# Performance work log

Measured on AMD Instinct MI355X. Metric: run time of the kernel, lower is better.

The kernel has to match this reference:

```python
import jax, jax.numpy as jnp
import numpy as np

WS = 7        # window size (square)
SH = 3        # shift size
NH = 8        # num heads
N = WS * WS   # tokens per window


def _rel_pos_index():
    coords = np.stack(np.meshgrid(np.arange(WS), np.arange(WS), indexing='ij'))
    cf = coords.reshape(2, -1)                      # (2, N)
    rel = cf[:, :, None] - cf[:, None, :]           # (2, N, N)
    rel = rel.transpose(1, 2, 0)
    rel[:, :, 0] += WS - 1
    rel[:, :, 1] += WS - 1
    rel[:, :, 0] *= 2 * WS - 1
    return rel.sum(-1)                              # (N, N) int


def _attn_mask(pH, pW):
    img = np.zeros((pH, pW), dtype=np.float32)
    h_sl = [(0, pH - WS), (pH - WS, pH - SH), (pH - SH, pH)]
    w_sl = [(0, pW - WS), (pW - WS, pW - SH), (pW - SH, pW)]
    cnt = 0
    for h0, h1 in h_sl:
        for w0, w1 in w_sl:
            img[h0:h1, w0:w1] = cnt
            cnt += 1
    m = img.reshape(pH // WS, WS, pW // WS, WS).transpose(0, 2, 1, 3).reshape(-1, N)
    diff = m[:, None, :] - m[:, :, None]            # (nw, N, N)
    return np.where(diff != 0, -100.0, 0.0).astype(np.float32)


def setup_inputs() -> dict:
    key = jax.random.key(0)
    ks = jax.random.split(key, 6)
    C = 256
    return {
        'x': jax.random.normal(ks[0], (32, 56, 56, C), dtype=jnp.float32),
        'qkv_weight': jax.random.normal(ks[1], (3 * C, C), dtype=jnp.float32) * 0.02,
        'qkv_bias': jax.random.normal(ks[2], (3 * C,), dtype=jnp.float32) * 0.02,
        'proj_weight': jax.random.normal(ks[3], (C, C), dtype=jnp.float32) * 0.02,
        'proj_bias': jax.random.normal(ks[4], (C,), dtype=jnp.float32) * 0.02,
        'rpb_table': jax.random.normal(ks[5], ((2 * WS - 1) ** 2, NH), dtype=jnp.float32) * 0.02,
    }


def reference(x, qkv_weight, qkv_bias, proj_weight, proj_bias, rpb_table):
    B, H, W, C = x.shape
    hd = C // NH
    pad_r = (WS - W % WS) % WS
    pad_b = (WS - H % WS) % WS
    xp = jnp.pad(x, ((0, 0), (0, pad_b), (0, pad_r), (0, 0)))
    pH, pW = H + pad_b, W + pad_r
    xp = jnp.roll(xp, shift=(-SH, -SH), axis=(1, 2))
    nw = (pH // WS) * (pW // WS)
    # window partition -> (B*nw, N, C)
    xw = xp.reshape(B, pH // WS, WS, pW // WS, WS, C)
    xw = xw.transpose(0, 1, 3, 2, 4, 5).reshape(B * nw, N, C)
    # qkv projection
    qkv = xw @ qkv_weight.T + qkv_bias                      # (B*nw, N, 3C)
    qkv = qkv.reshape(B * nw, N, 3, NH, hd).transpose(2, 0, 3, 1, 4)
    q, k, v = qkv[0], qkv[1], qkv[2]                        # (B*nw, NH, N, hd)
    q = q * (hd ** -0.5)
    attn = jnp.einsum('bhnd,bhmd->bhnm', q, k)              # (B*nw, NH, N, N)
    # relative position bias
    idx = jnp.asarray(_rel_pos_index())
    bias = rpb_table[idx].transpose(2, 0, 1)                # (NH, N, N)
    attn = attn + bias[None]
    # shift mask
    mask = jnp.asarray(_attn_mask(pH, pW))                  # (nw, N, N)
    attn = attn.reshape(B, nw, NH, N, N) + mask[None, :, None]
    attn = jax.nn.softmax(attn.reshape(B * nw, NH, N, N), axis=-1)
    out = jnp.einsum('bhnm,bhmd->bhnd', attn, v)            # (B*nw, NH, N, hd)
    out = out.transpose(0, 2, 1, 3).reshape(B * nw, N, C)
    out = out @ proj_weight.T + proj_bias
    # window reverse
    out = out.reshape(B, pH // WS, pW // WS, WS, WS, C)
    out = out.transpose(0, 1, 3, 2, 4, 5).reshape(B, pH, pW, C)
    out = jnp.roll(out, shift=(SH, SH), axis=(1, 2))
    return out[:, :H, :W, :]
```

## Files before the change

### kernel.cpp

```cpp
#include <hip/hip_runtime.h>
#include <hip/hip_bf16.h>

typedef __attribute__((ext_vector_type(4))) float f32x4;
typedef __attribute__((ext_vector_type(8))) short s16x8;
typedef __attribute__((ext_vector_type(4))) short s16x4;
typedef __attribute__((ext_vector_type(4))) unsigned uintx4;

#define LBS 264
#define VTS 72
#define LOS 132

__device__ __forceinline__ unsigned cvt2bf(float a, float b) {
    unsigned r;
    asm("v_cvt_pk_bf16_f32 %0, %1, %2" : "=v"(r) : "v"(a), "v"(b));
    return r;
}

__device__ __forceinline__ s16x4 pk4bf(float a, float b, float c, float d) {
    uint2 t = { cvt2bf(a, b), cvt2bf(c, d) };
    return __builtin_bit_cast(s16x4, t);
}

__device__ __forceinline__ s16x8 expand_z(s16x4 c) {
    uint2 u = __builtin_bit_cast(uint2, c);
    uintx4 r = { u.x & 0xFFFFu, u.x >> 16, u.y & 0xFFFFu, u.y >> 16 };
    return __builtin_bit_cast(s16x8, r);
}

__global__ void wcvt_kernel(const float* __restrict__ qw, const float* __restrict__ pw,
                            short* __restrict__ wqkv, short* __restrict__ wproj) {
    int idx = blockIdx.x * blockDim.x + threadIdx.x;
    int stride = gridDim.x * blockDim.x;
    for (int i = idx; i < 65536; i += stride) {
        const float* src = (i < 49152) ? (qw + i * 4) : (pw + (i - 49152) * 4);
        unsigned* dst = (unsigned*)((i < 49152) ? (wqkv + i * 4) : (wproj + (i - 49152) * 4));
        const f32x4 v = *(const f32x4*)src;
        uint2 o = { cvt2bf(v.x, v.y), cvt2bf(v.z, v.w) };
        *(uint2*)dst = o;
    }
}

__global__ void bmgen_kernel(const float* __restrict__ rpb, float* __restrict__ bm) {
    int idx = blockIdx.x * blockDim.x + threadIdx.x;
    if (idx >= 131072) return;
    int j = idx & 63;
    int i = (idx >> 6) & 63;
    int h = (idx >> 12) & 7;
    int c = idx >> 15;
    int cy = c >> 1, cx = c & 1;
    float v;
    if (j >= 49) {
        v = -1e9f;
    } else {
        int ic = i > 48 ? 48 : i;
        int yi = ic / 7, xi = ic % 7;
        int yj = j / 7, xj = j % 7;
        float bias = rpb[((yi - yj + 6) * 13 + (xi - xj + 6)) * 8 + h];
        int ri = (cy ? (yi < 4 ? 1 : 2) : 0) * 3 + (cx ? (xi < 4 ? 1 : 2) : 0);
        int rj = (cy ? (yj < 4 ? 1 : 2) : 0) * 3 + (cx ? (xj < 4 ? 1 : 2) : 0);
        float mask = (ri != rj) ? -100.0f : 0.0f;
        v = (bias + mask) * 1.4426950408889634f;
    }
    bm[idx] = v;
}

__global__ __launch_bounds__(512, 4)
void attn_kernel(const float* __restrict__ x,
                 const float* __restrict__ qkv_bias,
                 const short* __restrict__ wqkv,
                 const float* __restrict__ bm,
                 unsigned short* __restrict__ la) {
    __shared__ __align__(16) short buf[64 * LBS];
    __shared__ __align__(16) short lvt[128 * VTS];
    __shared__ float lml[4 * 64];

    const int tid  = threadIdx.x;
    const int w    = tid >> 6;
    const int lane = tid & 63;
    const int il   = lane & 15;
    const int gl   = lane >> 4;
    const int hl   = w >> 1;
    const int jh   = w & 1;

    const int hg  = blockIdx.x & 1;
    const int win = blockIdx.x >> 1;
    const int wid = win & 63;
    const int b   = win >> 6;
    const int wy  = wid >> 3, wx = wid & 7;

    {
        const int t0 = tid >> 3;
        const int cb = (tid & 7) << 2;
        const float* xrow = x;
        if (t0 < 49) {
            int ty = t0 / 7, tx = t0 % 7;
            int R = wy * 7 + ty + 3; if (R >= 56) R -= 56;
            int C = wx * 7 + tx + 3; if (C >= 56) C -= 56;
            xrow = x + (((b * 56 + R) * 56 + C) << 8);
        }
        #pragma unroll
        for (int j = 0; j < 8; j++) {
            int c4 = cb + 32 * j;
            uint2 o = { 0u, 0u };
            if (t0 < 49) {
                const f32x4 v = *(const f32x4*)(xrow + c4);
                o.x = cvt2bf(v.x, v.y); o.y = cvt2bf(v.z, v.w);
            }
            *(uint2*)&buf[t0 * LBS + c4] = o;
        }
    }
    __syncthreads();

    const int cls = ((wy == 7) ? 2 : 0) + ((wx == 7) ? 1 : 0);
    const float* bmp = bm + ((cls * 8 + hg * 4 + hl) * 64) * 64;
    f32x4 s[2][4];

    {
        f32x4 acc[4][3];
        #pragma unroll
        for (int mi = 0; mi < 4; mi++)
            #pragma unroll
            for (int t = 0; t < 3; t++) acc[mi][t] = (f32x4){0.f, 0.f, 0.f, 0.f};
        for (int k0 = 0; k0 < 256; k0 += 32) {
            s16x8 a[4];
            #pragma unroll
            for (int mi = 0; mi < 4; mi++)
                a[mi] = *(const s16x8*)&buf[(mi * 16 + il) * LBS + k0 + 8 * gl];
            #pragma unroll
            for (int t = 0; t < 3; t++) {
                s16x8 bfr = *(const s16x8*)(wqkv + (t * 256 + hg * 128 + 16 * w + il) * 256 + k0 + 8 * gl);
                #pragma unroll
                for (int mi = 0; mi < 4; mi++)
                    acc[mi][t] = __builtin_amdgcn_mfma_f32_16x16x32_bf16(a[mi], bfr, acc[mi][t], 0, 0, 0);
            }
        }
        {
            float bv = qkv_bias[512 + hg * 128 + 16 * w + il];
            #pragma unroll
            for (int mi = 0; mi < 4; mi++)
                *(s16x4*)&lvt[(16 * w + il) * VTS + mi * 16 + gl * 4] =
                    pk4bf(acc[mi][2][0] + bv, acc[mi][2][1] + bv,
                          acc[mi][2][2] + bv, acc[mi][2][3] + bv);
        }
        __syncthreads();
        {
            const float QSCL = 0.17677669529663687f * 1.4426950408889634f;
            float bq_ = qkv_bias[hg * 128 + 16 * w + il];
            float bk_ = qkv_bias[256 + hg * 128 + 16 * w + il];
            #pragma unroll
            for (int mi = 0; mi < 4; mi++)
                #pragma unroll
                for (int r = 0; r < 4; r++) {
                    int row = mi * 16 + gl * 4 + r;
                    unsigned u = cvt2bf((acc[mi][0][r] + bq_) * QSCL, acc[mi][1][r] + bk_);
                    buf[row * LBS + 16 * w + il] = (short)u;
                    buf[row * LBS + 128 + 16 * w + il] = (short)(u >> 16);
                }
        }
    }
    #pragma unroll
    for (int mi = 0; mi < 2; mi++)
        #pragma unroll
        for (int ni = 0; ni < 4; ni++)
            s[mi][ni] = *(const f32x4*)&bmp[(ni * 16 + il) * 64 + jh * 32 + mi * 16 + gl * 4];
    __syncthreads();

    {
        s16x8 bq[4];
        #pragma unroll
        for (int ni = 0; ni < 4; ni++)
            bq[ni] = *(const s16x8*)&buf[(ni * 16 + il) * LBS + hl * 32 + 8 * gl];
        #pragma unroll
        for (int mi = 0; mi < 2; mi++) {
            s16x8 ak = *(const s16x8*)&buf[(jh * 32 + mi * 16 + il) * LBS + 128 + hl * 32 + 8 * gl];
            #pragma unroll
            for (int ni = 0; ni < 4; ni++)
                s[mi][ni] = __builtin_amdgcn_mfma_f32_16x16x32_bf16(ak, bq[ni], s[mi][ni], 0, 0, 0);
        }
    }
    float l[4] = { 0.f, 0.f, 0.f, 0.f };
    s16x4 pkd[2][4];
    #pragma unroll
    for (int mi = 0; mi < 2; mi++)
        #pragma unroll
        for (int ni = 0; ni < 4; ni++) {
            float p0 = exp2f(s[mi][ni][0]);
            float p1 = exp2f(s[mi][ni][1]);
            float p2 = exp2f(s[mi][ni][2]);
            float p3 = exp2f(s[mi][ni][3]);
            l[ni] += (p0 + p1) + (p2 + p3);
            pkd[mi][ni] = pk4bf(p0, p1, p2, p3);
        }
    #pragma unroll
    for (int ni = 0; ni < 4; ni++) {
        l[ni] += __shfl_xor(l[ni], 16);
        l[ni] += __shfl_xor(l[ni], 32);
    }
    if (jh == 0 && gl == 0) {
        #pragma unroll
        for (int ni = 0; ni < 4; ni++) lml[hl * 64 + ni * 16 + il] = l[ni];
    }
    __syncthreads();

    f32x4 o[2][4];
    #pragma unroll
    for (int md = 0; md < 2; md++)
        #pragma unroll
        for (int ni = 0; ni < 4; ni++) o[md][ni] = (f32x4){0.f, 0.f, 0.f, 0.f};
    #pragma unroll
    for (int mi = 0; mi < 2; mi++) {
        s16x8 av[2];
        #pragma unroll
        for (int md = 0; md < 2; md++)
            av[md] = expand_z(*(const s16x4*)&lvt[(hl * 32 + md * 16 + il) * VTS + jh * 32 + mi * 16 + 4 * gl]);
        #pragma unroll
        for (int ni = 0; ni < 4; ni++) {
            s16x8 bp = expand_z(pkd[mi][ni]);
            #pragma unroll
            for (int md = 0; md < 2; md++)
                o[md][ni] = __builtin_amdgcn_mfma_f32_16x16x32_bf16(av[md], bp, o[md][ni], 0, 0, 0);
        }
    }
    float* lout = (float*)buf;
    if (jh == 0) {
        #pragma unroll
        for (int md = 0; md < 2; md++)
            #pragma unroll
            for (int ni = 0; ni < 4; ni++)
                *(f32x4*)&lout[(ni * 16 + il) * LOS + hl * 32 + md * 16 + gl * 4] = o[md][ni];
    }
    __syncthreads();
    if (jh == 1) {
        float sc[4];
        #pragma unroll
        for (int ni = 0; ni < 4; ni++)
            sc[ni] = __builtin_amdgcn_rcpf(l[ni] + lml[hl * 64 + ni * 16 + il]);
        #pragma unroll
        for (int ni = 0; ni < 4; ni++) {
            int i = ni * 16 + il;
            if (i < 49) {
                #pragma unroll
                for (int md = 0; md < 2; md++) {
                    f32x4 t = *(const f32x4*)&lout[i * LOS + hl * 32 + md * 16 + gl * 4];
                    uint2 pk = { cvt2bf((t.x + o[md][ni][0]) * sc[ni], (t.y + o[md][ni][1]) * sc[ni]),
                                 cvt2bf((t.z + o[md][ni][2]) * sc[ni], (t.w + o[md][ni][3]) * sc[ni]) };
                    *(uint2*)&la[(win * 49 + i) * 256 + hg * 128 + hl * 32 + md * 16 + gl * 4] = pk;
                }
            }
        }
    }
}

__global__ __launch_bounds__(512, 4)
void proj_kernel(const unsigned short* __restrict__ la,
                 const float* __restrict__ proj_bias,
                 const short* __restrict__ wproj,
                 float* __restrict__ out) {
    __shared__ __align__(16) short buf[64 * LBS];

    const int tid  = threadIdx.x;
    const int w    = tid >> 6;
    const int lane = tid & 63;
    const int il   = lane & 15;
    const int gl   = lane >> 4;

    const int win = blockIdx.x;
    const int wid = win & 63;
    const int b   = win >> 6;
    const int wy  = wid >> 3, wx = wid & 7;

    for (int i = tid; i < 2048; i += 512) {
        int t = i >> 5, c8 = (i & 31) << 3;
        uintx4 v = (t < 49) ? *(const uintx4*)&la[(win * 49 + t) * 256 + c8]
                            : (uintx4){0u, 0u, 0u, 0u};
        *(uintx4*)&buf[t * LBS + c8] = v;
    }
    __syncthreads();

    f32x4 acc[4][2];
    #pragma unroll
    for (int mi = 0; mi < 4; mi++)
        #pragma unroll
        for (int ni = 0; ni < 2; ni++) acc[mi][ni] = (f32x4){0.f, 0.f, 0.f, 0.f};
    for (int k0 = 0; k0 < 256; k0 += 32) {
        s16x8 a[4];
        #pragma unroll
        for (int mi = 0; mi < 4; mi++)
            a[mi] = *(const s16x8*)&buf[(mi * 16 + il) * LBS + k0 + 8 * gl];
        #pragma unroll
        for (int ni = 0; ni < 2; ni++) {
            s16x8 bw = *(const s16x8*)(wproj + (32 * w + 16 * ni + il) * 256 + k0 + 8 * gl);
            #pragma unroll
            for (int mi = 0; mi < 4; mi++)
                acc[mi][ni] = __builtin_amdgcn_mfma_f32_16x16x32_bf16(a[mi], bw, acc[mi][ni], 0, 0, 0);
        }
    }
    __syncthreads();
    #pragma unroll
    for (int ni = 0; ni < 2; ni++) {
        int oc = 32 * w + 16 * ni + il;
        float pb = proj_bias[oc];
        #pragma unroll
        for (int mi = 0; mi < 4; mi++)
            #pragma unroll
            for (int r = 0; r < 4; r++) {
                int t = mi * 16 + gl * 4 + r;
                if (t < 49) {
                    unsigned u = cvt2bf(acc[mi][ni][r] + pb, 0.f);
                    buf[t * LBS + oc] = (short)u;
                }
            }
    }
    __syncthreads();
    for (int i = tid; i < 1568; i += 512) {
        int t = i >> 5, c8 = (i & 31) << 3;
        uintx4 u = *(const uintx4*)&buf[t * LBS + c8];
        f32x4 v0, v1;
        v0.x = __builtin_bit_cast(float, u.x << 16);
        v0.y = __builtin_bit_cast(float, u.x & 0xFFFF0000u);
        v0.z = __builtin_bit_cast(float, u.y << 16);
        v0.w = __builtin_bit_cast(float, u.y & 0xFFFF0000u);
        v1.x = __builtin_bit_cast(float, u.z << 16);
        v1.y = __builtin_bit_cast(float, u.z & 0xFFFF0000u);
        v1.z = __builtin_bit_cast(float, u.w << 16);
        v1.w = __builtin_bit_cast(float, u.w & 0xFFFF0000u);
        int ty = t / 7, tx = t % 7;
        int R = wy * 7 + ty + 3; if (R >= 56) R -= 56;
        int C = wx * 7 + tx + 3; if (C >= 56) C -= 56;
        float* op = out + (((b * 56 + R) * 56 + C) << 8) + c8;
        *(f32x4*)op = v0;
        *(f32x4*)(op + 4) = v1;
    }
}

extern "C" void kernel_launch(void* const* d_in, const int* in_sizes, int n_in,
                              void* d_out, int out_size, void* d_ws, size_t ws_size,
                              hipStream_t stream) {
    const float* x   = (const float*)d_in[0];
    const float* qw  = (const float*)d_in[1];
    const float* qb  = (const float*)d_in[2];
    const float* pw  = (const float*)d_in[3];
    const float* pb  = (const float*)d_in[4];
    const float* rpb = (const float*)d_in[5];

    short* wqkv  = (short*)d_ws;
    short* wproj = wqkv + 768 * 256;
    float* bmt   = (float*)((char*)d_ws + 524288);
    unsigned short* lat = (unsigned short*)((char*)d_ws + 2097152);

    wcvt_kernel<<<128, 256, 0, stream>>>(qw, pw, wqkv, wproj);
    bmgen_kernel<<<512, 256, 0, stream>>>(rpb, bmt);
    attn_kernel<<<4096, 512, 0, stream>>>(x, qb, wqkv, bmt, lat);
    proj_kernel<<<2048, 512, 0, stream>>>(lat, pb, wproj, (float*)d_out);
}
```

Baseline: 226.5 us.

## Load x directly into MFMA fragments, skip LDS staging, merge prep kernels

The QKV GEMM's A operand is now read straight from global fp32 x and converted to bf16 in registers, instead of first being staged through LDS. This removes the initial staging pass and two block barriers. The weight-convert and bias/mask-generation kernels are merged into one launch, and the QK^T fragment loads are reordered. In exchange, every wave now reloads the whole 49x256 window tile from global memory/cache, multiplying x read traffic per block.

```diff
diff --git a/kernel.cpp b/kernel.cpp
--- a/kernel.cpp
+++ b/kernel.cpp
@@ -27,41 +27,50 @@
     return __builtin_bit_cast(s16x8, r);
 }
 
-__global__ void wcvt_kernel(const float* __restrict__ qw, const float* __restrict__ pw,
-                            short* __restrict__ wqkv, short* __restrict__ wproj) {
+__device__ __forceinline__ s16x8 load_a(const float* rp, int off, bool valid) {
+    f32x4 v0 = { 0.f, 0.f, 0.f, 0.f }, v1 = { 0.f, 0.f, 0.f, 0.f };
+    if (valid) {
+        v0 = *(const f32x4*)(rp + off);
+        v1 = *(const f32x4*)(rp + off + 4);
+    }
+    uintx4 u = { cvt2bf(v0.x, v0.y), cvt2bf(v0.z, v0.w),
+                 cvt2bf(v1.x, v1.y), cvt2bf(v1.z, v1.w) };
+    return __builtin_bit_cast(s16x8, u);
+}
+
+__global__ void prep_kernel(const float* __restrict__ qw, const float* __restrict__ pw,
+                            const float* __restrict__ rpb,
+                            short* __restrict__ wqkv, short* __restrict__ wproj,
+                            float* __restrict__ bm) {
     int idx = blockIdx.x * blockDim.x + threadIdx.x;
-    int stride = gridDim.x * blockDim.x;
-    for (int i = idx; i < 65536; i += stride) {
-        const float* src = (i < 49152) ? (qw + i * 4) : (pw + (i - 49152) * 4);
-        unsigned* dst = (unsigned*)((i < 49152) ? (wqkv + i * 4) : (wproj + (i - 49152) * 4));
+    if (idx < 65536) {
+        const float* src = (idx < 49152) ? (qw + idx * 4) : (pw + (idx - 49152) * 4);
+        unsigned* dst = (unsigned*)((idx < 49152) ? (wqkv + idx * 4) : (wproj + (idx - 49152) * 4));
         const f32x4 v = *(const f32x4*)src;
         uint2 o = { cvt2bf(v.x, v.y), cvt2bf(v.z, v.w) };
         *(uint2*)dst = o;
-    }
-}
-
-__global__ void bmgen_kernel(const float* __restrict__ rpb, float* __restrict__ bm) {
-    int idx = blockIdx.x * blockDim.x + threadIdx.x;
-    if (idx >= 131072) return;
-    int j = idx & 63;
-    int i = (idx >> 6) & 63;
-    int h = (idx >> 12) & 7;
-    int c = idx >> 15;
-    int cy = c >> 1, cx = c & 1;
-    float v;
-    if (j >= 49) {
-        v = -1e9f;
     } else {
-        int ic = i > 48 ? 48 : i;
-        int yi = ic / 7, xi = ic % 7;
-        int yj = j / 7, xj = j % 7;
-        float bias = rpb[((yi - yj + 6) * 13 + (xi - xj + 6)) * 8 + h];
-        int ri = (cy ? (yi < 4 ? 1 : 2) : 0) * 3 + (cx ? (xi < 4 ? 1 : 2) : 0);
-        int rj = (cy ? (yj < 4 ? 1 : 2) : 0) * 3 + (cx ? (xj < 4 ? 1 : 2) : 0);
-        float mask = (ri != rj) ? -100.0f : 0.0f;
-        v = (bias + mask) * 1.4426950408889634f;
-    }
-    bm[idx] = v;
+        int k = idx - 65536;
+        int j = k & 63;
+        int i = (k >> 6) & 63;
+        int h = (k >> 12) & 7;
+        int c = k >> 15;
+        int cy = c >> 1, cx = c & 1;
+        float v;
+        if (j >= 49) {
+            v = -1e9f;
+        } else {
+            int ic = i > 48 ? 48 : i;
+            int yi = ic / 7, xi = ic % 7;
+            int yj = j / 7, xj = j % 7;
+            float bias = rpb[((yi - yj + 6) * 13 + (xi - xj + 6)) * 8 + h];
+            int ri = (cy ? (yi < 4 ? 1 : 2) : 0) * 3 + (cx ? (xi < 4 ? 1 : 2) : 0);
+            int rj = (cy ? (yj < 4 ? 1 : 2) : 0) * 3 + (cx ? (xj < 4 ? 1 : 2) : 0);
+            float mask = (ri != rj) ? -100.0f : 0.0f;
+            v = (bias + mask) * 1.4426950408889634f;
+        }
+        bm[k] = v;
+    }
 }
 
 __global__ __launch_bounds__(512, 4)
@@ -88,32 +97,17 @@
     const int b   = win >> 6;
     const int wy  = wid >> 3, wx = wid & 7;
 
-    {
-        const int t0 = tid >> 3;
-        const int cb = (tid & 7) << 2;
-        const float* xrow = x;
-        if (t0 < 49) {
-            int ty = t0 / 7, tx = t0 % 7;
-            int R = wy * 7 + ty + 3; if (R >= 56) R -= 56;
-            int C = wx * 7 + tx + 3; if (C >= 56) C -= 56;
-            xrow = x + (((b * 56 + R) * 56 + C) << 8);
-        }
-        #pragma unroll
-        for (int j = 0; j < 8; j++) {
-            int c4 = cb + 32 * j;
-            uint2 o = { 0u, 0u };
-            if (t0 < 49) {
-                const f32x4 v = *(const f32x4*)(xrow + c4);
-                o.x = cvt2bf(v.x, v.y); o.y = cvt2bf(v.z, v.w);
-            }
-            *(uint2*)&buf[t0 * LBS + c4] = o;
-        }
-    }
-    __syncthreads();
-
-    const int cls = ((wy == 7) ? 2 : 0) + ((wx == 7) ? 1 : 0);
-    const float* bmp = bm + ((cls * 8 + hg * 4 + hl) * 64) * 64;
-    f32x4 s[2][4];
+    const float* rp[4];
+    #pragma unroll
+    for (int mi = 0; mi < 4; mi++) {
+        int t = mi * 16 + il;
+        int tc = t > 48 ? 48 : t;
+        int ty = tc / 7, tx = tc % 7;
+        int R = wy * 7 + ty + 3; if (R >= 56) R -= 56;
+        int C = wx * 7 + tx + 3; if (C >= 56) C -= 56;
+        rp[mi] = x + (((b * 56 + R) * 56 + C) << 8);
+    }
+    const bool v3 = (il == 0);
 
     {
         f32x4 acc[4][3];
@@ -123,9 +117,10 @@
             for (int t = 0; t < 3; t++) acc[mi][t] = (f32x4){0.f, 0.f, 0.f, 0.f};
         for (int k0 = 0; k0 < 256; k0 += 32) {
             s16x8 a[4];
-            #pragma unroll
-            for (int mi = 0; mi < 4; mi++)
-                a[mi] = *(const s16x8*)&buf[(mi * 16 + il) * LBS + k0 + 8 * gl];
+            a[0] = load_a(rp[0], k0 + 8 * gl, true);
+            a[1] = load_a(rp[1], k0 + 8 * gl, true);
+            a[2] = load_a(rp[2], k0 + 8 * gl, true);
+            a[3] = load_a(rp[3], k0 + 8 * gl, v3);
             #pragma unroll
             for (int t = 0; t < 3; t++) {
                 s16x8 bfr = *(const s16x8*)(wqkv + (t * 256 + hg * 128 + 16 * w + il) * 256 + k0 + 8 * gl);
@@ -142,7 +137,6 @@
                     pk4bf(acc[mi][2][0] + bv, acc[mi][2][1] + bv,
                           acc[mi][2][2] + bv, acc[mi][2][3] + bv);
         }
-        __syncthreads();
         {
             const float QSCL = 0.17677669529663687f * 1.4426950408889634f;
             float bq_ = qkv_bias[hg * 128 + 16 * w + il];
@@ -158,6 +152,9 @@
                 }
         }
     }
+    const int cls = ((wy == 7) ? 2 : 0) + ((wx == 7) ? 1 : 0);
+    const float* bmp = bm + ((cls * 8 + hg * 4 + hl) * 64) * 64;
+    f32x4 s[2][4];
     #pragma unroll
     for (int mi = 0; mi < 2; mi++)
         #pragma unroll
@@ -166,16 +163,16 @@
     __syncthreads();
 
     {
-        s16x8 bq[4];
-        #pragma unroll
-        for (int ni = 0; ni < 4; ni++)
-            bq[ni] = *(const s16x8*)&buf[(ni * 16 + il) * LBS + hl * 32 + 8 * gl];
-        #pragma unroll
-        for (int mi = 0; mi < 2; mi++) {
-            s16x8 ak = *(const s16x8*)&buf[(jh * 32 + mi * 16 + il) * LBS + 128 + hl * 32 + 8 * gl];
-            #pragma unroll
-            for (int ni = 0; ni < 4; ni++)
-                s[mi][ni] = __builtin_amdgcn_mfma_f32_16x16x32_bf16(ak, bq[ni], s[mi][ni], 0, 0, 0);
+        s16x8 ak[2];
+        #pragma unroll
+        for (int mi = 0; mi < 2; mi++)
+            ak[mi] = *(const s16x8*)&buf[(jh * 32 + mi * 16 + il) * LBS + 128 + hl * 32 + 8 * gl];
+        #pragma unroll
+        for (int ni = 0; ni < 4; ni++) {
+            s16x8 bq = *(const s16x8*)&buf[(ni * 16 + il) * LBS + hl * 32 + 8 * gl];
+            #pragma unroll
+            for (int mi = 0; mi < 2; mi++)
+                s[mi][ni] = __builtin_amdgcn_mfma_f32_16x16x32_bf16(ak[mi], bq, s[mi][ni], 0, 0, 0);
         }
     }
     float l[4] = { 0.f, 0.f, 0.f, 0.f };
@@ -348,8 +345,7 @@
     float* bmt   = (float*)((char*)d_ws + 524288);
     unsigned short* lat = (unsigned short*)((char*)d_ws + 2097152);
 
-    wcvt_kernel<<<128, 256, 0, stream>>>(qw, pw, wqkv, wproj);
-    bmgen_kernel<<<512, 256, 0, stream>>>(rpb, bmt);
+    prep_kernel<<<768, 256, 0, stream>>>(qw, pw, rpb, wqkv, wproj, bmt);
     attn_kernel<<<4096, 512, 0, stream>>>(x, qb, wqkv, bmt, lat);
     proj_kernel<<<2048, 512, 0, stream>>>(lat, pb, wproj, (float*)d_out);
 }
```

After: 371.3 us. 63.9% more time.
